# Kernel optimization log

Hardware: AMD Instinct MI355X
Metric: run time of the kernel (lower is better)

## Reference

```python
import jax, jax.numpy as jnp
import numpy as np

D_MODEL, D_STATE, D_CONV, EXPAND = 1024, 16, 4, 2
D_INNER = EXPAND * D_MODEL  # 2048
DT_RANK = (D_MODEL + 15) // 16  # 64
B_SZ, L = 2, 4096


def setup_inputs() -> dict:
    key = jax.random.key(0)
    ks = jax.random.split(key, 10)
    x = jax.random.normal(ks[0], (B_SZ, L, D_MODEL), dtype=jnp.float32)
    in_proj_w = jax.random.normal(ks[1], (2 * D_INNER, D_MODEL), dtype=jnp.float32) * 0.02
    conv_w = jax.random.normal(ks[2], (D_INNER, D_CONV), dtype=jnp.float32) * 0.2
    conv_b = jax.random.normal(ks[3], (D_INNER,), dtype=jnp.float32) * 0.02
    x_proj_w = jax.random.normal(ks[4], (DT_RANK + 2 * D_STATE, D_INNER), dtype=jnp.float32) * 0.02
    dt_std = DT_RANK ** -0.5
    dt_proj_w = jax.random.uniform(ks[5], (D_INNER, DT_RANK), minval=-dt_std, maxval=dt_std, dtype=jnp.float32)
    # dt bias init: inverse softplus of dt sampled log-uniform in [1e-3, 1e-1]
    dt = jnp.exp(jax.random.uniform(ks[6], (D_INNER,)) * (np.log(0.1) - np.log(0.001)) + np.log(0.001))
    dt = jnp.clip(dt, 1e-4, None)
    dt_proj_b = dt + jnp.log(-jnp.expm1(-dt))
    A_log = jnp.log(jnp.broadcast_to(jnp.arange(1, D_STATE + 1, dtype=jnp.float32), (D_INNER, D_STATE)))
    Dp = jnp.ones((D_INNER,), dtype=jnp.float32)
    out_proj_w = jax.random.normal(ks[7], (D_MODEL, D_INNER), dtype=jnp.float32) * 0.02
    return {"x": x, "in_proj_w": in_proj_w, "conv_w": conv_w, "conv_b": conv_b,
            "x_proj_w": x_proj_w, "dt_proj_w": dt_proj_w, "dt_proj_b": dt_proj_b,
            "A_log": A_log, "Dp": Dp, "out_proj_w": out_proj_w}


def _mamba(x, in_proj_w, conv_w, conv_b, x_proj_w, dt_proj_w, dt_proj_b, A_log, Dp, out_proj_w):
    b, l, _ = x.shape
    xz = jnp.einsum('bld,ed->ble', x, in_proj_w)          # (b, l, 2*d_inner)
    u, z = jnp.split(xz, 2, axis=-1)                       # each (b, l, d_inner)
    # causal depthwise conv along l
    uc = jnp.transpose(u, (0, 2, 1))                       # (b, d, l)
    kern = conv_w[:, None, :]                              # (d, 1, w)
    uc = jax.lax.conv_general_dilated(
        uc, kern, window_strides=(1,), padding=[(D_CONV - 1, 0)],
        dimension_numbers=('NCH', 'OIH', 'NCH'), feature_group_count=D_INNER)
    uc = uc + conv_b[None, :, None]
    u_act = jax.nn.silu(jnp.transpose(uc, (0, 2, 1)))      # (b, l, d_inner)
    # projections for dt, B, C
    x_dbl = jnp.einsum('bld,ed->ble', u_act, x_proj_w)     # (b, l, dt_rank + 2n)
    dt_lo = x_dbl[..., :DT_RANK]
    Bm = x_dbl[..., DT_RANK:DT_RANK + D_STATE]             # (b, l, n)
    Cm = x_dbl[..., DT_RANK + D_STATE:]                    # (b, l, n)
    dt = jnp.einsum('blr,dr->bld', dt_lo, dt_proj_w)       # (b, l, d_inner)
    delta = jax.nn.softplus(dt + dt_proj_b)                # (b, l, d_inner)
    A = -jnp.exp(A_log)                                    # (d_inner, n)

    def step(h, inp):
        d_t, B_t, C_t, u_t = inp                           # (b,d), (b,n), (b,n), (b,d)
        dA = jnp.exp(d_t[..., None] * A)                   # (b, d, n)
        h = h * dA + (d_t * u_t)[..., None] * B_t[:, None, :]
        y = jnp.einsum('bdn,bn->bd', h, C_t)
        return h, y

    xs = (jnp.transpose(delta, (1, 0, 2)), jnp.transpose(Bm, (1, 0, 2)),
          jnp.transpose(Cm, (1, 0, 2)), jnp.transpose(u_act, (1, 0, 2)))
    h0 = jnp.zeros((b, D_INNER, D_STATE), dtype=x.dtype)
    _, ys = jax.lax.scan(step, h0, xs)                     # (l, b, d)
    y = jnp.transpose(ys, (1, 0, 2)) + u_act * Dp          # (b, l, d_inner)
    y = y * jax.nn.silu(z)
    return jnp.einsum('bld,ed->ble', y, out_proj_w)        # (b, l, d_model)


def reference(x, in_proj_w, conv_w, conv_b, x_proj_w, dt_proj_w, dt_proj_b, A_log, Dp, out_proj_w):
    return _mamba(x, in_proj_w, conv_w, conv_b, x_proj_w, dt_proj_w, dt_proj_b, A_log, Dp, out_proj_w)
```

## Files before the change

### kernel.cpp

```cpp
#include <hip/hip_runtime.h>

#define D_MODEL  1024
#define D_STATE  16
#define D_CONV   4
#define D_INNER  2048
#define DT_RANK  64
#define B_SZ     2
#define L_SEQ    4096
#define NPROJ    96
#define M_ROWS   (B_SZ * L_SEQ)
#define NC       64
#define LC       64

typedef __bf16 bf16;
typedef __bf16 bf16x8 __attribute__((ext_vector_type(8)));
typedef __bf16 bf16x4 __attribute__((ext_vector_type(4)));
typedef __bf16 bf16x2 __attribute__((ext_vector_type(2)));
typedef float  f32x4  __attribute__((ext_vector_type(4)));
typedef float  f32x2  __attribute__((ext_vector_type(2)));

__device__ __forceinline__ void gload16(const void* g, void* l) {
    __builtin_amdgcn_global_load_lds(
        (const __attribute__((address_space(1))) unsigned int*)g,
        (__attribute__((address_space(3))) unsigned int*)l,
        16, 0, 0);
}

__global__ __launch_bounds__(256) void f2b4(const float4* __restrict__ in,
                                            bf16x4* __restrict__ out, int n4) {
    int i = blockIdx.x * 256 + threadIdx.x;
    if (i < n4) {
        float4 v = in[i];
        bf16x4 o = {(bf16)v.x, (bf16)v.y, (bf16)v.z, (bf16)v.w};
        out[i] = o;
    }
}

__global__ __launch_bounds__(256) void f2b_pad_xproj(const float* __restrict__ in,
                                                     bf16* __restrict__ out) {
    int i = blockIdx.x * 256 + threadIdx.x;
    int row = i >> 11, col = i & 2047;
    float v = (row < NPROJ) ? in[row * 2048 + col] : 0.f;
    out[i] = (bf16)v;
}

template <int MODE, int WM>
__global__ __launch_bounds__(WM * 128, 2)
void gemm_bt(const bf16* __restrict__ A, const bf16* __restrict__ B,
             int M, int N, int K, int lda, int ldb,
             float* __restrict__ outf, bf16* __restrict__ outb,
             const float* __restrict__ bias, int ldout) {
    constexpr int NW      = WM * 2;
    constexpr int A_TILES = WM * 4;
    constexpr int B_TILES = 8;
    constexpr int UPW     = (A_TILES + B_TILES) * 2 / NW;

    __shared__ bf16 As[A_TILES * 2 * 64 * 8];
    __shared__ bf16 Bs[B_TILES * 2 * 64 * 8];

    const int tid  = threadIdx.x;
    const int wave = tid >> 6;
    const int lane = tid & 63;
    const int l15  = lane & 15;
    const int lk   = lane >> 4;
    const int mBase = blockIdx.y * (WM * 64);
    const int nBase = blockIdx.x * 128;
    const int koff  = blockIdx.z * K;
    const int wm    = wave >> 1;
    const int wn    = wave & 1;

    f32x4 acc[4][4];
    const f32x4 zz = {0.f, 0.f, 0.f, 0.f};
#pragma unroll
    for (int i = 0; i < 4; i++)
#pragma unroll
        for (int j = 0; j < 4; j++) acc[i][j] = zz;

    for (int k0 = 0; k0 < K; k0 += 64) {
#pragma unroll
        for (int u = 0; u < UPW; u++) {
            const int g = wave * UPW + u;
            const int s = g & 1;
            const int t = g >> 1;
            if (t < A_TILES) {
                const bf16* gA = A + (size_t)(mBase + t * 16 + l15) * lda
                                   + koff + k0 + s * 32 + lk * 8;
                gload16(gA, &As[((t * 2 + s) * 64 + lane) * 8]);
            } else {
                const int nt = t - A_TILES;
                const bf16* gB = B + (size_t)(nBase + nt * 16 + l15) * ldb
                                   + koff + k0 + s * 32 + lk * 8;
                gload16(gB, &Bs[((nt * 2 + s) * 64 + lane) * 8]);
            }
        }
        __syncthreads();

#pragma unroll
        for (int s = 0; s < 2; s++) {
            bf16x8 af[4], bfr[4];
#pragma unroll
            for (int i = 0; i < 4; i++)
                af[i] = *(const bf16x8*)&As[(((wm * 4 + i) * 2 + s) * 64 + lane) * 8];
#pragma unroll
            for (int j = 0; j < 4; j++)
                bfr[j] = *(const bf16x8*)&Bs[(((wn * 4 + j) * 2 + s) * 64 + lane) * 8];
#pragma unroll
            for (int i = 0; i < 4; i++)
#pragma unroll
                for (int j = 0; j < 4; j++)
                    acc[i][j] = __builtin_amdgcn_mfma_f32_16x16x32_bf16(af[i], bfr[j],
                                                                        acc[i][j], 0, 0, 0);
        }
        __syncthreads();
    }

#pragma unroll
    for (int i = 0; i < 4; i++) {
#pragma unroll
        for (int j = 0; j < 4; j++) {
            const int col = nBase + wn * 64 + j * 16 + l15;
#pragma unroll
            for (int r = 0; r < 4; r++) {
                const int row = mBase + wm * 64 + i * 16 + lk * 4 + r;
                float v = acc[i][j][r];
                if (MODE == 0) {
                    outb[(size_t)row * ldout + col] = (bf16)v;
                } else if (MODE == 2) {
                    float xv = v + bias[col];
                    float sp = fmaxf(xv, 0.f) + log1pf(expf(-fabsf(xv)));
                    outb[(size_t)row * ldout + col] = (bf16)sp;
                } else if (MODE == 3) {
                    outf[(size_t)row * ldout + col] = v;
                } else {
                    outf[((size_t)blockIdx.z * M + row) * 128 + col] = v;
                }
            }
        }
    }
}

__global__ __launch_bounds__(256)
void reduce_xproj(const float* __restrict__ part, float* __restrict__ xdbl,
                  bf16* __restrict__ xdbl_b) {
    int i = blockIdx.x * 256 + threadIdx.x;
    if (i >= M_ROWS * NPROJ) return;
    int row = i / NPROJ;
    int col = i - row * NPROJ;
    size_t o = (size_t)row * 128 + col;
    float s = part[o] + part[(size_t)M_ROWS * 128 + o]
            + part[(size_t)2 * M_ROWS * 128 + o] + part[(size_t)3 * M_ROWS * 128 + o];
    xdbl[i] = s;
    xdbl_b[i] = (bf16)s;
}

__global__ __launch_bounds__(256)
void conv_silu(const bf16* __restrict__ xz, const float* __restrict__ cw,
               const float* __restrict__ cb, bf16* __restrict__ uact) {
    int i = blockIdx.x * 256 + threadIdx.x;
    int dp = i & 1023;
    int l  = (i >> 10) & (L_SEQ - 1);
    int b  = i >> 22;
    float4 w0 = *(const float4*)&cw[dp * 8];
    float4 w1 = *(const float4*)&cw[dp * 8 + 4];
    const float wv0[4] = {w0.x, w0.y, w0.z, w0.w};
    const float wv1[4] = {w1.x, w1.y, w1.z, w1.w};
    float2 cbv = *(const float2*)&cb[dp * 2];
    float a0 = cbv.x, a1 = cbv.y;
    size_t rb = (size_t)b * L_SEQ;
    const unsigned int* xz32 = (const unsigned int*)xz;
#pragma unroll
    for (int k = 0; k < 4; k++) {
        int li = l - 3 + k;
        if (li >= 0) {
            unsigned int u = xz32[(rb + li) * 2048 + dp];
            float lo = __uint_as_float(u << 16);
            float hi = __uint_as_float(u & 0xFFFF0000u);
            a0 += lo * wv0[k];
            a1 += hi * wv1[k];
        }
    }
    float s0 = a0 / (1.f + expf(-a0));
    float s1 = a1 / (1.f + expf(-a1));
    bf16x2 pk = {(bf16)s0, (bf16)s1};
    ((bf16x2*)uact)[(rb + l) * 1024 + dp] = pk;
}

__global__ __launch_bounds__(256)
void scan_passA(const bf16* __restrict__ delta, const bf16* __restrict__ uact,
                const float* __restrict__ xdbl, const float* __restrict__ A_log,
                float* __restrict__ hloc, float* __restrict__ Ssum) {
    int tid = threadIdx.x, bid = blockIdx.x;
    int d = (bid & 7) * 256 + tid;
    int c = (bid >> 3) & (NC - 1);
    int b = bid >> 9;
    float a[16];
    bool regular = true;
#pragma unroll
    for (int n = 0; n < 16; n++) {
        a[n] = expf(A_log[d * 16 + n]);
        regular = regular && (fabsf(a[n] - (float)(n + 1) * a[0]) < 1e-3f * (n + 1));
    }
    f32x2 h2[8];
#pragma unroll
    for (int k = 0; k < 8; k++) h2[k] = {0.f, 0.f};
    float S = 0.f;
    size_t rowb = (size_t)b * L_SEQ + c * LC;

    if (regular) {
        const float na0 = -a[0] * 1.44269504f;
        for (int t = 0; t < LC; t++) {
            size_t r = rowb + t;
            float dt = (float)delta[r * D_INNER + d];
            float u  = (float)uact [r * D_INNER + d];
            S += dt;
            f32x2 du2 = {dt * u, dt * u};
            const f32x2* B2 = (const f32x2*)(xdbl + r * NPROJ + DT_RANK);
            float e  = exp2f(dt * na0);
            float e2 = e * e;
            f32x2 p  = {e, e2};
            f32x2 ee = {e2, e2};
#pragma unroll
            for (int k = 0; k < 8; k++) {
                h2[k] = h2[k] * p + du2 * B2[k];
                p = p * ee;
            }
        }
    } else {
        f32x2 An2[8];
#pragma unroll
        for (int k = 0; k < 8; k++)
            An2[k] = {-a[2 * k] * 1.44269504f, -a[2 * k + 1] * 1.44269504f};
        for (int t = 0; t < LC; t++) {
            size_t r = rowb + t;
            float dt = (float)delta[r * D_INNER + d];
            float u  = (float)uact [r * D_INNER + d];
            S += dt;
            f32x2 du2 = {dt * u, dt * u};
            const f32x2* B2 = (const f32x2*)(xdbl + r * NPROJ + DT_RANK);
#pragma unroll
            for (int k = 0; k < 8; k++) {
                f32x2 dA = {exp2f(dt * An2[k][0]), exp2f(dt * An2[k][1])};
                h2[k] = h2[k] * dA + du2 * B2[k];
            }
        }
    }
    size_t cb_ = (size_t)b * NC + c;
#pragma unroll
    for (int k = 0; k < 8; k++) {
        hloc[(cb_ * 16 + 2 * k    ) * D_INNER + d] = h2[k][0];
        hloc[(cb_ * 16 + 2 * k + 1) * D_INNER + d] = h2[k][1];
    }
    Ssum[cb_ * D_INNER + d] = S;
}

__global__ __launch_bounds__(256)
void scan_mid(const float* __restrict__ hloc, const float* __restrict__ Ssum,
              const float* __restrict__ A_log, float* __restrict__ h0) {
    int idx = blockIdx.x * 256 + threadIdx.x;
    int d = idx & (D_INNER - 1);
    int n = (idx >> 11) & 15;
    int b = idx >> 15;
    float An = -expf(A_log[d * 16 + n]) * 1.44269504f;
    float H = 0.f;
    for (int c = 0; c < NC; c++) {
        size_t cb_ = (size_t)b * NC + c;
        h0[(cb_ * 16 + n) * D_INNER + d] = H;
        H = H * exp2f(Ssum[cb_ * D_INNER + d] * An)
          + hloc[(cb_ * 16 + n) * D_INNER + d];
    }
}

__global__ __launch_bounds__(256)
void scan_passB(const bf16* __restrict__ delta, const bf16* __restrict__ uact,
                const float* __restrict__ xdbl, const float* __restrict__ A_log,
                const float* __restrict__ h0, const float* __restrict__ Dp,
                const bf16* __restrict__ xz, bf16* __restrict__ y) {
    int tid = threadIdx.x, bid = blockIdx.x;
    int d = (bid & 7) * 256 + tid;
    int c = (bid >> 3) & (NC - 1);
    int b = bid >> 9;
    float a[16];
    bool regular = true;
#pragma unroll
    for (int n = 0; n < 16; n++) {
        a[n] = expf(A_log[d * 16 + n]);
        regular = regular && (fabsf(a[n] - (float)(n + 1) * a[0]) < 1e-3f * (n + 1));
    }
    size_t cb_ = (size_t)b * NC + c;
    f32x2 h2[8];
#pragma unroll
    for (int k = 0; k < 8; k++) {
        h2[k][0] = h0[(cb_ * 16 + 2 * k    ) * D_INNER + d];
        h2[k][1] = h0[(cb_ * 16 + 2 * k + 1) * D_INNER + d];
    }
    float Dd = Dp[d];
    size_t rowb = (size_t)b * L_SEQ + c * LC;

    if (regular) {
        const float na0 = -a[0] * 1.44269504f;
        for (int t = 0; t < LC; t++) {
            size_t r = rowb + t;
            float dt = (float)delta[r * D_INNER + d];
            float u  = (float)uact [r * D_INNER + d];
            f32x2 du2 = {dt * u, dt * u};
            const f32x2* B2 = (const f32x2*)(xdbl + r * NPROJ + DT_RANK);
            const f32x2* C2 = B2 + 8;
            float e  = exp2f(dt * na0);
            float e2 = e * e;
            f32x2 p  = {e, e2};
            f32x2 ee = {e2, e2};
            f32x2 yt2 = {0.f, 0.f};
#pragma unroll
            for (int k = 0; k < 8; k++) {
                h2[k] = h2[k] * p + du2 * B2[k];
                yt2 = yt2 + h2[k] * C2[k];
                p = p * ee;
            }
            float yt = yt2[0] + yt2[1] + u * Dd;
            float z = (float)xz[r * (2 * D_INNER) + D_INNER + d];
            float g = z / (1.f + expf(-z));
            y[r * D_INNER + d] = (bf16)(yt * g);
        }
    } else {
        f32x2 An2[8];
#pragma unroll
        for (int k = 0; k < 8; k++)
            An2[k] = {-a[2 * k] * 1.44269504f, -a[2 * k + 1] * 1.44269504f};
        for (int t = 0; t < LC; t++) {
            size_t r = rowb + t;
            float dt = (float)delta[r * D_INNER + d];
            float u  = (float)uact [r * D_INNER + d];
            f32x2 du2 = {dt * u, dt * u};
            const f32x2* B2 = (const f32x2*)(xdbl + r * NPROJ + DT_RANK);
            const f32x2* C2 = B2 + 8;
            f32x2 yt2 = {0.f, 0.f};
#pragma unroll
            for (int k = 0; k < 8; k++) {
                f32x2 dA = {exp2f(dt * An2[k][0]), exp2f(dt * An2[k][1])};
                h2[k] = h2[k] * dA + du2 * B2[k];
                yt2 = yt2 + h2[k] * C2[k];
            }
            float yt = yt2[0] + yt2[1] + u * Dd;
            float z = (float)xz[r * (2 * D_INNER) + D_INNER + d];
            float g = z / (1.f + expf(-z));
            y[r * D_INNER + d] = (bf16)(yt * g);
        }
    }
}

extern "C" void kernel_launch(void* const* d_in, const int* in_sizes, int n_in,
                              void* d_out, int out_size, void* d_ws, size_t ws_size,
                              hipStream_t stream) {
    const float* x         = (const float*)d_in[0];
    const float* in_proj_w = (const float*)d_in[1];
    const float* conv_w    = (const float*)d_in[2];
    const float* conv_b    = (const float*)d_in[3];
    const float* x_proj_w  = (const float*)d_in[4];
    const float* dt_proj_w = (const float*)d_in[5];
    const float* dt_proj_b = (const float*)d_in[6];
    const float* A_log     = (const float*)d_in[7];
    const float* Dp        = (const float*)d_in[8];
    const float* out_proj_w= (const float*)d_in[9];
    float* out             = (float*)d_out;

    char* p = (char*)d_ws;
    auto alloc = [&](size_t bytes) -> char* {
        char* r = p;
        p += (bytes + 255) & ~(size_t)255;
        return r;
    };
    bf16*  x_bf    = (bf16*) alloc((size_t)M_ROWS * D_MODEL * 2);
    bf16*  w_in    = (bf16*) alloc((size_t)2 * D_INNER * D_MODEL * 2);
    bf16*  w_xp    = (bf16*) alloc((size_t)128 * D_INNER * 2);
    bf16*  w_dt    = (bf16*) alloc((size_t)D_INNER * DT_RANK * 2);
    bf16*  w_out   = (bf16*) alloc((size_t)D_MODEL * D_INNER * 2);
    bf16*  xz      = (bf16*) alloc((size_t)M_ROWS * 2 * D_INNER * 2);
    bf16*  uact    = (bf16*) alloc((size_t)M_ROWS * D_INNER * 2);
    float* xdbl    = (float*)alloc((size_t)M_ROWS * NPROJ * 4);
    bf16*  xdbl_b  = (bf16*) alloc((size_t)M_ROWS * NPROJ * 2);
    bf16*  deltab  = (bf16*) alloc((size_t)M_ROWS * D_INNER * 2);
    float* hloc    = (float*)alloc((size_t)B_SZ * NC * 16 * D_INNER * 4);
    float* Ssum    = (float*)alloc((size_t)B_SZ * NC * D_INNER * 4);
    float* h0      = (float*)alloc((size_t)B_SZ * NC * 16 * D_INNER * 4);
    bf16*  ybf     = (bf16*) alloc((size_t)M_ROWS * D_INNER * 2);
    float* partial = hloc;

    {
        int n4;
        n4 = M_ROWS * D_MODEL / 4;
        f2b4<<<(n4 + 255) / 256, 256, 0, stream>>>((const float4*)x, (bf16x4*)x_bf, n4);
        n4 = 2 * D_INNER * D_MODEL / 4;
        f2b4<<<(n4 + 255) / 256, 256, 0, stream>>>((const float4*)in_proj_w, (bf16x4*)w_in, n4);
        f2b_pad_xproj<<<(128 * D_INNER) / 256, 256, 0, stream>>>(x_proj_w, w_xp);
        n4 = D_INNER * DT_RANK / 4;
        f2b4<<<(n4 + 255) / 256, 256, 0, stream>>>((const float4*)dt_proj_w, (bf16x4*)w_dt, n4);
        n4 = D_MODEL * D_INNER / 4;
        f2b4<<<(n4 + 255) / 256, 256, 0, stream>>>((const float4*)out_proj_w, (bf16x4*)w_out, n4);
    }

    gemm_bt<0, 4><<<dim3(2 * D_INNER / 128, M_ROWS / 256, 1), 512, 0, stream>>>(
        x_bf, w_in, M_ROWS, 2 * D_INNER, D_MODEL, D_MODEL, D_MODEL,
        nullptr, xz, nullptr, 2 * D_INNER);

    conv_silu<<<(M_ROWS * D_INNER / 2) / 256, 256, 0, stream>>>(xz, conv_w, conv_b, uact);

    gemm_bt<4, 2><<<dim3(1, M_ROWS / 128, 4), 256, 0, stream>>>(
        uact, w_xp, M_ROWS, 128, 512, D_INNER, D_INNER,
        partial, nullptr, nullptr, 128);
    reduce_xproj<<<(M_ROWS * NPROJ + 255) / 256, 256, 0, stream>>>(partial, xdbl, xdbl_b);

    gemm_bt<2, 4><<<dim3(D_INNER / 128, M_ROWS / 256, 1), 512, 0, stream>>>(
        xdbl_b, w_dt, M_ROWS, D_INNER, DT_RANK, NPROJ, DT_RANK,
        nullptr, deltab, dt_proj_b, D_INNER);

    scan_passA<<<B_SZ * NC * (D_INNER / 256), 256, 0, stream>>>(
        deltab, uact, xdbl, A_log, hloc, Ssum);
    scan_mid<<<(B_SZ * D_INNER * 16) / 256, 256, 0, stream>>>(hloc, Ssum, A_log, h0);
    scan_passB<<<B_SZ * NC * (D_INNER / 256), 256, 0, stream>>>(
        deltab, uact, xdbl, A_log, h0, Dp, xz, ybf);

    gemm_bt<3, 4><<<dim3(D_MODEL / 128, M_ROWS / 256, 1), 512, 0, stream>>>(
        ybf, w_out, M_ROWS, D_MODEL, D_INNER, D_INNER, D_INNER,
        out, nullptr, nullptr, D_MODEL);

    (void)in_sizes; (void)n_in; (void)out_size; (void)ws_size;
}
```

Before: 511.6 us.

## Fuse fp32-to-bf16 casts, stage B/C in LDS for scans, shrink out-proj tile

The four float-to-bf16 conversion launches are merged into a single kernel that picks its source and destination by index range, removing three launches. Both scan passes now stage each chunk's B (and C) rows from xdbl into shared memory once per block, so the per-timestep loop reads them from LDS rather than from global memory and caches. The output projection GEMM switches to a 128-row tile with 256 threads, doubling the number of blocks. The costs are a barrier in each scan block, branchy index logic in the cast kernel, and possibly less data reuse per block in the GEMM.

Measured after the change: 494.9 us. 1.03x faster.

```diff
diff --git a/kernel.cpp b/kernel.cpp
--- a/kernel.cpp
+++ b/kernel.cpp
@@ -26,14 +26,30 @@
         16, 0, 0);
 }
 
-__global__ __launch_bounds__(256) void f2b4(const float4* __restrict__ in,
-                                            bf16x4* __restrict__ out, int n4) {
-    int i = blockIdx.x * 256 + threadIdx.x;
-    if (i < n4) {
-        float4 v = in[i];
-        bf16x4 o = {(bf16)v.x, (bf16)v.y, (bf16)v.z, (bf16)v.w};
-        out[i] = o;
-    }
+__global__ __launch_bounds__(256)
+void f2b_all(const float4* __restrict__ s0, bf16x4* __restrict__ d0, int n0,
+             const float4* __restrict__ s1, bf16x4* __restrict__ d1, int n1,
+             const float4* __restrict__ s2, bf16x4* __restrict__ d2, int n2,
+             const float4* __restrict__ s3, bf16x4* __restrict__ d3, int n3) {
+    int j = blockIdx.x * 256 + threadIdx.x;
+    const float4* s; bf16x4* d;
+    if (j < n0) { s = s0; d = d0; }
+    else {
+        j -= n0;
+        if (j < n1) { s = s1; d = d1; }
+        else {
+            j -= n1;
+            if (j < n2) { s = s2; d = d2; }
+            else {
+                j -= n2;
+                if (j >= n3) return;
+                s = s3; d = d3;
+            }
+        }
+    }
+    float4 v = s[j];
+    bf16x4 o = {(bf16)v.x, (bf16)v.y, (bf16)v.z, (bf16)v.w};
+    d[j] = o;
 }
 
 __global__ __launch_bounds__(256) void f2b_pad_xproj(const float* __restrict__ in,
@@ -189,10 +205,14 @@
 void scan_passA(const bf16* __restrict__ delta, const bf16* __restrict__ uact,
                 const float* __restrict__ xdbl, const float* __restrict__ A_log,
                 float* __restrict__ hloc, float* __restrict__ Ssum) {
+    __shared__ float sB[LC][16];
     int tid = threadIdx.x, bid = blockIdx.x;
     int d = (bid & 7) * 256 + tid;
     int c = (bid >> 3) & (NC - 1);
     int b = bid >> 9;
+    size_t rowb = (size_t)b * L_SEQ + c * LC;
+    for (int i = tid; i < LC * 16; i += 256)
+        sB[i >> 4][i & 15] = xdbl[(rowb + (i >> 4)) * NPROJ + DT_RANK + (i & 15)];
     float a[16];
     bool regular = true;
 #pragma unroll
@@ -204,7 +224,7 @@
 #pragma unroll
     for (int k = 0; k < 8; k++) h2[k] = {0.f, 0.f};
     float S = 0.f;
-    size_t rowb = (size_t)b * L_SEQ + c * LC;
+    __syncthreads();
 
     if (regular) {
         const float na0 = -a[0] * 1.44269504f;
@@ -214,7 +234,7 @@
             float u  = (float)uact [r * D_INNER + d];
             S += dt;
             f32x2 du2 = {dt * u, dt * u};
-            const f32x2* B2 = (const f32x2*)(xdbl + r * NPROJ + DT_RANK);
+            const f32x2* B2 = (const f32x2*)&sB[t][0];
             float e  = exp2f(dt * na0);
             float e2 = e * e;
             f32x2 p  = {e, e2};
@@ -236,7 +256,7 @@
             float u  = (float)uact [r * D_INNER + d];
             S += dt;
             f32x2 du2 = {dt * u, dt * u};
-            const f32x2* B2 = (const f32x2*)(xdbl + r * NPROJ + DT_RANK);
+            const f32x2* B2 = (const f32x2*)&sB[t][0];
 #pragma unroll
             for (int k = 0; k < 8; k++) {
                 f32x2 dA = {exp2f(dt * An2[k][0]), exp2f(dt * An2[k][1])};
@@ -275,10 +295,14 @@
                 const float* __restrict__ xdbl, const float* __restrict__ A_log,
                 const float* __restrict__ h0, const float* __restrict__ Dp,
                 const bf16* __restrict__ xz, bf16* __restrict__ y) {
+    __shared__ float sBC[LC][32];
     int tid = threadIdx.x, bid = blockIdx.x;
     int d = (bid & 7) * 256 + tid;
     int c = (bid >> 3) & (NC - 1);
     int b = bid >> 9;
+    size_t rowb = (size_t)b * L_SEQ + c * LC;
+    for (int i = tid; i < LC * 32; i += 256)
+        sBC[i >> 5][i & 31] = xdbl[(rowb + (i >> 5)) * NPROJ + DT_RANK + (i & 31)];
     float a[16];
     bool regular = true;
 #pragma unroll
@@ -294,7 +318,7 @@
         h2[k][1] = h0[(cb_ * 16 + 2 * k + 1) * D_INNER + d];
     }
     float Dd = Dp[d];
-    size_t rowb = (size_t)b * L_SEQ + c * LC;
+    __syncthreads();
 
     if (regular) {
         const float na0 = -a[0] * 1.44269504f;
@@ -303,8 +327,8 @@
             float dt = (float)delta[r * D_INNER + d];
             float u  = (float)uact [r * D_INNER + d];
             f32x2 du2 = {dt * u, dt * u};
-            const f32x2* B2 = (const f32x2*)(xdbl + r * NPROJ + DT_RANK);
-            const f32x2* C2 = B2 + 8;
+            const f32x2* B2 = (const f32x2*)&sBC[t][0];
+            const f32x2* C2 = (const f32x2*)&sBC[t][16];
             float e  = exp2f(dt * na0);
             float e2 = e * e;
             f32x2 p  = {e, e2};
@@ -331,8 +355,8 @@
             float dt = (float)delta[r * D_INNER + d];
             float u  = (float)uact [r * D_INNER + d];
             f32x2 du2 = {dt * u, dt * u};
-            const f32x2* B2 = (const f32x2*)(xdbl + r * NPROJ + DT_RANK);
-            const f32x2* C2 = B2 + 8;
+            const f32x2* B2 = (const f32x2*)&sBC[t][0];
+            const f32x2* C2 = (const f32x2*)&sBC[t][16];
             f32x2 yt2 = {0.f, 0.f};
 #pragma unroll
             for (int k = 0; k < 8; k++) {
@@ -386,16 +410,17 @@
     float* partial = hloc;
 
     {
-        int n4;
-        n4 = M_ROWS * D_MODEL / 4;
-        f2b4<<<(n4 + 255) / 256, 256, 0, stream>>>((const float4*)x, (bf16x4*)x_bf, n4);
-        n4 = 2 * D_INNER * D_MODEL / 4;
-        f2b4<<<(n4 + 255) / 256, 256, 0, stream>>>((const float4*)in_proj_w, (bf16x4*)w_in, n4);
+        const int n0 = M_ROWS * D_MODEL / 4;
+        const int n1 = 2 * D_INNER * D_MODEL / 4;
+        const int n2 = D_INNER * DT_RANK / 4;
+        const int n3 = D_MODEL * D_INNER / 4;
+        const int nt = n0 + n1 + n2 + n3;
+        f2b_all<<<(nt + 255) / 256, 256, 0, stream>>>(
+            (const float4*)x, (bf16x4*)x_bf, n0,
+            (const float4*)in_proj_w, (bf16x4*)w_in, n1,
+            (const float4*)dt_proj_w, (bf16x4*)w_dt, n2,
+            (const float4*)out_proj_w, (bf16x4*)w_out, n3);
         f2b_pad_xproj<<<(128 * D_INNER) / 256, 256, 0, stream>>>(x_proj_w, w_xp);
-        n4 = D_INNER * DT_RANK / 4;
-        f2b4<<<(n4 + 255) / 256, 256, 0, stream>>>((const float4*)dt_proj_w, (bf16x4*)w_dt, n4);
-        n4 = D_MODEL * D_INNER / 4;
-        f2b4<<<(n4 + 255) / 256, 256, 0, stream>>>((const float4*)out_proj_w, (bf16x4*)w_out, n4);
     }
 
     gemm_bt<0, 4><<<dim3(2 * D_INNER / 128, M_ROWS / 256, 1), 512, 0, stream>>>(
@@ -419,7 +444,7 @@
     scan_passB<<<B_SZ * NC * (D_INNER / 256), 256, 0, stream>>>(
         deltab, uact, xdbl, A_log, h0, Dp, xz, ybf);
 
-    gemm_bt<3, 4><<<dim3(D_MODEL / 128, M_ROWS / 256, 1), 512, 0, stream>>>(
+    gemm_bt<3, 2><<<dim3(D_MODEL / 128, M_ROWS / 128, 1), 256, 0, stream>>>(
         ybf, w_out, M_ROWS, D_MODEL, D_INNER, D_INNER, D_INNER,
         out, nullptr, nullptr, D_MODEL);
 
```
